# Kernel optimization log

Measured on AMD Instinct MI355X. Metric: run time of the kernel, lower is better.

Reference implementation:

```python
import jax, jax.numpy as jnp
import numpy as np

D_MODEL = 768
N_HEADS = 12
D_FF = 3072
EPS = 1e-6


def _xavier(key, shape):
    fan_out, fan_in = shape
    a = jnp.sqrt(6.0 / (fan_in + fan_out))
    return jax.random.uniform(key, shape, jnp.float32, -a, a)


def setup_inputs() -> dict:
    key = jax.random.key(0)
    ks = jax.random.split(key, 10)
    B, S = 2, 2048
    x = jax.random.normal(ks[0], (B, S, D_MODEL), jnp.float32)
    mask = jax.random.randint(ks[1], (B, 1, 1, S), 0, 2) == 1
    wq = _xavier(ks[2], (D_MODEL, D_MODEL)); bq = jnp.zeros((D_MODEL,))
    wk = _xavier(ks[3], (D_MODEL, D_MODEL)); bk = jnp.zeros((D_MODEL,))
    wv = _xavier(ks[4], (D_MODEL, D_MODEL)); bv = jnp.zeros((D_MODEL,))
    wo = _xavier(ks[5], (D_MODEL, D_MODEL)); bo = jnp.zeros((D_MODEL,))
    w1 = _xavier(ks[6], (D_FF, D_MODEL)); b1 = jnp.zeros((D_FF,))
    w2 = _xavier(ks[7], (D_MODEL, D_FF)); b2 = jnp.zeros((D_MODEL,))
    g1 = jnp.ones((D_MODEL,)); be1 = jnp.zeros((D_MODEL,))
    g2 = jnp.ones((D_MODEL,)); be2 = jnp.zeros((D_MODEL,))
    return dict(x=x, mask=mask, wq=wq, bq=bq, wk=wk, bk=bk, wv=wv, bv=bv,
                wo=wo, bo=bo, w1=w1, b1=b1, w2=w2, b2=b2,
                g1=g1, be1=be1, g2=g2, be2=be2)


def _layer_norm(x, gamma, beta):
    # torch: mean + unbiased std (ddof=1), divide by (std + eps)
    mean = jnp.mean(x, axis=-1, keepdims=True)
    std = jnp.std(x, axis=-1, keepdims=True, ddof=1)
    return gamma * (x - mean) / (std + EPS) + beta


def _encoder(x, mask, wq, bq, wk, bk, wv, bv, wo, bo, w1, b1, w2, b2, g1, be1, g2, be2):
    B, S, D = x.shape
    H, Dk = N_HEADS, D // N_HEADS
    q = (x @ wq.T + bq).reshape(B, S, H, Dk).transpose(0, 2, 1, 3)
    k = (x @ wk.T + bk).reshape(B, S, H, Dk).transpose(0, 2, 1, 3)
    v = (x @ wv.T + bv).reshape(B, S, H, Dk).transpose(0, 2, 1, 3)
    scores = jnp.einsum('bhqd,bhkd->bhqk', q, k) / jnp.sqrt(jnp.float32(Dk))
    scores = jnp.where(mask, jnp.float32(-1e9), scores)
    probs = jax.nn.softmax(scores, axis=-1)
    attn = jnp.einsum('bhqk,bhkd->bhqd', probs, v)
    attn = attn.transpose(0, 2, 1, 3).reshape(B, S, D)
    attn = attn @ wo.T + bo
    x = _layer_norm(x + attn, g1, be1)
    ff = jax.nn.relu(x @ w1.T + b1) @ w2.T + b2
    return _layer_norm(x + ff, g2, be2)


def reference(x, mask, wq, bq, wk, bk, wv, bv, wo, bo, w1, b1, w2, b2, g1, be1, g2, be2):
    return _encoder(x, mask, wq, bq, wk, bk, wv, bv, wo, bo, w1, b1, w2, b2, g1, be1, g2, be2)
```

## Files before the change

kernel.cpp:

```cpp
#include <hip/hip_runtime.h>
#include <hip/hip_bf16.h>

typedef __hip_bfloat16 bf16;
typedef unsigned short ushort;
typedef __attribute__((ext_vector_type(8))) short short8;
typedef __attribute__((ext_vector_type(4))) float f32x4;

__device__ __forceinline__ float b2f(bf16 h) { return __bfloat162float(h); }
__device__ __forceinline__ bf16 f2b(float f) { return __float2bfloat16(f); }
__device__ __forceinline__ ushort f2bu(float f) {
    bf16 t = __float2bfloat16(f);
    ushort u;
    __builtin_memcpy(&u, &t, 2);
    return u;
}
__device__ __forceinline__ float bits2f(unsigned int u16) {
    unsigned int v = u16 << 16;
    float f;
    __builtin_memcpy(&f, &v, 4);
    return f;
}

__device__ __forceinline__ void gload16(const void* g, void* l) {
    __builtin_amdgcn_global_load_lds(
        (const __attribute__((address_space(1))) void*)g,
        (__attribute__((address_space(3))) void*)l, 16, 0, 0);
}

__global__ void detect_dtype_kernel(const unsigned short* __restrict__ x,
                                    int* __restrict__ flag) {
    __shared__ int cnt;
    if (threadIdx.x == 0) cnt = 0;
    __syncthreads();
    int local = 0;
    for (int i = threadIdx.x; i < 2048; i += 256) {
        float v = bits2f((unsigned int)x[i]);
        if (!(fabsf(v) < 1e4f)) local++;
    }
    atomicAdd(&cnt, local);
    __syncthreads();
    if (threadIdx.x == 0) flag[0] = (cnt >= 8) ? 1 : 0;
}

__device__ __forceinline__ void load8f_rt(const void* p, int isf, float* f) {
    if (isf) {
        const float* q = (const float*)p;
        float4 a = *(const float4*)q;
        float4 b = *(const float4*)(q + 4);
        f[0] = a.x; f[1] = a.y; f[2] = a.z; f[3] = a.w;
        f[4] = b.x; f[5] = b.y; f[6] = b.z; f[7] = b.w;
    } else {
        uint4 u = *(const uint4*)p;
        f[0] = bits2f(u.x & 0xffffu); f[1] = bits2f(u.x >> 16);
        f[2] = bits2f(u.y & 0xffffu); f[3] = bits2f(u.y >> 16);
        f[4] = bits2f(u.z & 0xffffu); f[5] = bits2f(u.z >> 16);
        f[6] = bits2f(u.w & 0xffffu); f[7] = bits2f(u.w >> 16);
    }
}
__device__ __forceinline__ float loadf_rt(const void* p, int isf, size_t i) {
    return isf ? ((const float*)p)[i] : bits2f(((const ushort*)p)[i]);
}

__global__ __launch_bounds__(256) void conv_all_k(
    const int* __restrict__ dflag,
    const void* __restrict__ x,
    const void* __restrict__ wq, const void* __restrict__ wk,
    const void* __restrict__ wv, const void* __restrict__ wo,
    const void* __restrict__ w1, const void* __restrict__ w2,
    const void* __restrict__ bq, const void* __restrict__ bk,
    const void* __restrict__ bv, const void* __restrict__ bo,
    const void* __restrict__ b1, const void* __restrict__ b2,
    const void* __restrict__ g1, const void* __restrict__ be1,
    const void* __restrict__ g2, const void* __restrict__ be2,
    ushort* __restrict__ xb, ushort* __restrict__ wall,
    float* __restrict__ vall)
{
    const int isf = dflag[0];
    const int esz = isf ? 4 : 2;
    const int gt = blockIdx.x * 256 + threadIdx.x;
    const int stride = gridDim.x * 256;

    for (int v = gt; v < 393216; v += stride) {
        float f[8];
        load8f_rt((const char*)x + (size_t)v * 8 * esz, isf, f);
        unsigned int wd[4];
        #pragma unroll
        for (int i = 0; i < 4; ++i)
            wd[i] = (unsigned int)f2bu(f[2 * i]) | ((unsigned int)f2bu(f[2 * i + 1]) << 16);
        *(uint4*)(xb + (size_t)v * 8) = make_uint4(wd[0], wd[1], wd[2], wd[3]);
    }
    for (int v = gt; v < 884736; v += stride) {
        const void* src; int loc;
        if (v < 73728)        { src = wq; loc = v; }
        else if (v < 147456)  { src = wk; loc = v - 73728; }
        else if (v < 221184)  { src = wv; loc = v - 147456; }
        else if (v < 294912)  { src = wo; loc = v - 221184; }
        else if (v < 589824)  { src = w1; loc = v - 294912; }
        else                  { src = w2; loc = v - 589824; }
        float f[8];
        load8f_rt((const char*)src + (size_t)loc * 8 * esz, isf, f);
        unsigned int wd[4];
        #pragma unroll
        for (int i = 0; i < 4; ++i)
            wd[i] = (unsigned int)f2bu(f[2 * i]) | ((unsigned int)f2bu(f[2 * i + 1]) << 16);
        *(uint4*)(wall + (size_t)v * 8) = make_uint4(wd[0], wd[1], wd[2], wd[3]);
    }
    for (int i = gt; i < 9984; i += stride) {
        const void* s; int l;
        if (i < 768)       { s = bq;  l = i; }
        else if (i < 1536) { s = bk;  l = i - 768; }
        else if (i < 2304) { s = bv;  l = i - 1536; }
        else if (i < 3072) { s = bo;  l = i - 2304; }
        else if (i < 6144) { s = b1;  l = i - 3072; }
        else if (i < 6912) { s = b2;  l = i - 6144; }
        else if (i < 7680) { s = g1;  l = i - 6912; }
        else if (i < 8448) { s = be1; l = i - 7680; }
        else if (i < 9216) { s = g2;  l = i - 8448; }
        else               { s = be2; l = i - 9216; }
        vall[i] = loadf_rt(s, isf, l);
    }
}

template <int BM>
__device__ __forceinline__ void gemm_bf16_body(
    const ushort* __restrict__ A, const ushort* __restrict__ Bw,
    const float* __restrict__ bias, ushort* __restrict__ Cb,
    float* __restrict__ Cf, int N, int K, int bm, int bn, int relu)
{
    __shared__ __align__(16) ushort As[2][BM][64];
    __shared__ __align__(16) ushort Bs[2][128][64];
    const int tid = threadIdx.x;
    const int w = tid >> 6, lane = tid & 63;
    const int quad = lane >> 4, l15 = lane & 15;
    constexpr int FM = BM / 32;
    const int wr = (w >> 1) * (BM / 2), wc = (w & 1) * 64;

    constexpr int CA = (BM * 128) / 4096;
    constexpr int CB = 4;
    size_t aoff[CA]; int albase[CA];
    #pragma unroll
    for (int c = 0; c < CA; ++c) {
        int byte = c * 4096 + tid * 16;
        int row = byte >> 7, colb = byte & 127;
        int csrc = colb ^ ((row & 7) << 4);
        aoff[c] = (size_t)(bm + row) * K + (csrc >> 1);
        albase[c] = c * 4096 + w * 1024;
    }
    size_t boff[CB]; int blbase[CB];
    #pragma unroll
    for (int c = 0; c < CB; ++c) {
        int byte = c * 4096 + tid * 16;
        int row = byte >> 7, colb = byte & 127;
        int csrc = colb ^ ((row & 7) << 4);
        boff[c] = (size_t)(bn + row) * K + (csrc >> 1);
        blbase[c] = c * 4096 + w * 1024;
    }

    f32x4 acc[FM][4];
    #pragma unroll
    for (int i = 0; i < FM; ++i)
        #pragma unroll
        for (int j = 0; j < 4; ++j) acc[i][j] = (f32x4){0.f, 0.f, 0.f, 0.f};

    constexpr int ASZ = BM * 128;
    constexpr int BSZ = 128 * 128;

#define STAGE(buf, k0)                                                        \
    {                                                                         \
        char* ab = (char*)As + (buf) * ASZ;                                   \
        char* bb = (char*)Bs + (buf) * BSZ;                                   \
        _Pragma("unroll")                                                     \
        for (int c = 0; c < CA; ++c)                                          \
            gload16(A + aoff[c] + (k0), ab + albase[c]);                      \
        _Pragma("unroll")                                                     \
        for (int c = 0; c < CB; ++c)                                          \
            gload16(Bw + boff[c] + (k0), bb + blbase[c]);                     \
    }

    const int NT = K >> 6;
    STAGE(0, 0);
    int cur = 0;
    for (int t = 0; t < NT; ++t) {
        __syncthreads();
        if (t + 1 < NT) STAGE(cur ^ 1, (t + 1) * 64);

        const ushort (*Asb)[64] = As[cur];
        const ushort (*Bsb)[64] = Bs[cur];
        short8 af[FM][2], bfr[4][2];
        #pragma unroll
        for (int i = 0; i < FM; ++i) {
            int r = wr + i * 16 + l15;
            int sw = (r & 7) << 3;
            af[i][0] = *(const short8*)&Asb[r][(quad * 8) ^ sw];
            af[i][1] = *(const short8*)&Asb[r][(32 + quad * 8) ^ sw];
        }
        #pragma unroll
        for (int j = 0; j < 4; ++j) {
            int r = wc + j * 16 + l15;
            int sw = (r & 7) << 3;
            bfr[j][0] = *(const short8*)&Bsb[r][(quad * 8) ^ sw];
            bfr[j][1] = *(const short8*)&Bsb[r][(32 + quad * 8) ^ sw];
        }
        #pragma unroll
        for (int h = 0; h < 2; ++h)
            #pragma unroll
            for (int i = 0; i < FM; ++i)
                #pragma unroll
                for (int j = 0; j < 4; ++j)
                    acc[i][j] = __builtin_amdgcn_mfma_f32_16x16x32_bf16(
                        af[i][h], bfr[j][h], acc[i][j], 0, 0, 0);
        cur ^= 1;
    }
#undef STAGE

    #pragma unroll
    for (int j = 0; j < 4; ++j) {
        int col = bn + wc + j * 16 + l15;
        float bv = bias[col];
        #pragma unroll
        for (int i = 0; i < FM; ++i) {
            int row0 = bm + wr + i * 16 + quad * 4;
            #pragma unroll
            for (int r = 0; r < 4; ++r) {
                float vv = acc[i][j][r] + bv;
                if (relu) vv = fmaxf(vv, 0.f);
                size_t idx = (size_t)(row0 + r) * N + col;
                if (Cb) Cb[idx] = f2bu(vv);
                if (Cf) Cf[idx] = vv;
            }
        }
    }
}

__device__ __forceinline__ int xcd_swz(int bid, int nwg) {
    int cpx = nwg >> 3;
    return (bid & 7) * cpx + (bid >> 3);
}

template <int BM>
__global__ __launch_bounds__(256) void gemm_b(
    const ushort* __restrict__ A, const ushort* __restrict__ Bw,
    const float* __restrict__ bias, ushort* __restrict__ Cb,
    float* __restrict__ Cf, int N, int K, int relu)
{
    int nwg = gridDim.x * gridDim.y;
    int bid = xcd_swz(blockIdx.y * gridDim.x + blockIdx.x, nwg);
    int bx = bid % gridDim.x, by = bid / gridDim.x;
    gemm_bf16_body<BM>(A, Bw, bias, Cb, Cf, N, K, by * BM, bx * 128, relu);
}

__global__ __launch_bounds__(256) void gemm_qkv_b(
    const ushort* __restrict__ x, const ushort* __restrict__ wall,
    const float* __restrict__ vall,
    ushort* __restrict__ qb, ushort* __restrict__ kb, ushort* __restrict__ vb)
{
    int bid = xcd_swz(blockIdx.y * 18 + blockIdx.x, 576);
    int bx = bid % 18, by = bid / 18;
    const int mat = bx / 6;
    const int bn = (bx % 6) * 128;
    const ushort* W = wall + (size_t)mat * 589824;
    const float* Bi = vall + mat * 768;
    ushort* O = (mat == 0) ? qb : (mat == 1) ? kb : vb;
    gemm_bf16_body<128>(x, W, Bi, O, nullptr, 768, 768, by * 128, bn, 0);
}

__global__ __launch_bounds__(512) void attn_mfma_b(
    const ushort* __restrict__ q, const ushort* __restrict__ k,
    const ushort* __restrict__ v, const int* __restrict__ mask,
    float* __restrict__ opart, float* __restrict__ mlbuf)
{
    const int S = 2048, D = 768;
    const size_t NXD = 3145728;
    const float SC2 = 0.125f * 1.44269504088896f;
    __shared__ __align__(16) ushort Ks[64][72];
    __shared__ __align__(16) ushort Vt[64][72];
    __shared__ __align__(16) ushort Ps[8][16][72];
    __shared__ float mkAll[1024];

    const int tid = threadIdx.x;
    const int w = tid >> 6, lane = tid & 63;
    const int quad = lane >> 4, l15 = lane & 15;

    const int bx = blockIdx.x;
    const int part = bx / 384;
    const int rest = bx - part * 384;
    const int q0 = (rest & 15) * 128;
    const int h = (rest >> 4) % 12;
    const int b = rest / 192;
    const int kbase = part * 1024;

    #pragma unroll
    for (int i = 0; i < 2; ++i) {
        int idx = tid + i * 512;
        mkAll[idx] = mask[b * S + kbase + idx] ? -30000.f : 0.f;
    }

    const size_t qrow = (size_t)(b * S + q0 + w * 16 + l15) * D + h * 64;
    const short8 aQ0 = *(const short8*)&q[qrow + quad * 8];
    const short8 aQ1 = *(const short8*)&q[qrow + 32 + quad * 8];

    short8 ones;
    #pragma unroll
    for (int j = 0; j < 8; ++j) ones[j] = (short)0x3F80;

    f32x4 o[4], lacc;
    #pragma unroll
    for (int i = 0; i < 4; ++i) o[i] = (f32x4){0.f, 0.f, 0.f, 0.f};
    lacc = (f32x4){0.f, 0.f, 0.f, 0.f};
    float m_run = -3.0e38f;

    const int sr = tid >> 3;
    const int sc0 = (tid & 7) * 8;

    const ushort* kp = k + (size_t)(b * S + kbase + sr) * D + h * 64 + sc0;
    const ushort* vp = v + (size_t)(b * S + kbase + lane) * D + h * 64 + w * 8;
    uint4 ka = *(const uint4*)kp;
    uint4 va = *(const uint4*)vp;

    for (int kt = 0; kt < 16; ++kt) {
        __syncthreads();
        *(uint4*)&Ks[sr][sc0] = ka;
        {
            alignas(16) ushort tmp[8];
            *(uint4*)tmp = va;
            #pragma unroll
            for (int i = 0; i < 8; ++i) Vt[w * 8 + i][lane] = tmp[i];
        }
        __syncthreads();

        if (kt + 1 < 16) {
            kp += 64 * D;
            vp += 64 * D;
            ka = *(const uint4*)kp;
            va = *(const uint4*)vp;
        }

        const float* mk = &mkAll[kt * 64];
        float scv[4][4];
        float vm = -3.0e38f;
        __builtin_amdgcn_s_setprio(1);
        #pragma unroll
        for (int s = 0; s < 4; ++s) {
            short8 bk0 = *(const short8*)&Ks[s * 16 + l15][quad * 8];
            short8 bk1 = *(const short8*)&Ks[s * 16 + l15][32 + quad * 8];
            f32x4 c = (f32x4){0.f, 0.f, 0.f, 0.f};
            c = __builtin_amdgcn_mfma_f32_16x16x32_bf16(aQ0, bk0, c, 0, 0, 0);
            c = __builtin_amdgcn_mfma_f32_16x16x32_bf16(aQ1, bk1, c, 0, 0, 0);
            float mb = mk[s * 16 + l15];
            #pragma unroll
            for (int r = 0; r < 4; ++r) {
                float val = __builtin_fmaf(c[r], SC2, mb);
                scv[s][r] = val;
                vm = fmaxf(vm, val);
            }
        }
        __builtin_amdgcn_s_setprio(0);
        vm = fmaxf(vm, __shfl_xor(vm, 1, 16));
        vm = fmaxf(vm, __shfl_xor(vm, 2, 16));
        vm = fmaxf(vm, __shfl_xor(vm, 4, 16));
        vm = fmaxf(vm, __shfl_xor(vm, 8, 16));

        if (__any(vm > m_run + 11.0f)) {
            float mn = fmaxf(m_run, vm);
            float alpha = exp2f(m_run - mn);
            #pragma unroll
            for (int s = 0; s < 4; ++s) o[s] *= alpha;
            lacc *= alpha;
            m_run = mn;
        }

        #pragma unroll
        for (int r = 0; r < 4; ++r)
            #pragma unroll
            for (int s = 0; s < 4; ++s)
                Ps[w][quad * 4 + r][(s * 16 + l15) ^ (quad << 4)] =
                    f2bu(exp2f(scv[s][r] - m_run));
        asm volatile("s_waitcnt lgkmcnt(0)" ::: "memory");

        {
            const int pswz = (l15 >> 2) << 4;
            short8 aP0 = *(const short8*)&Ps[w][l15][(quad * 8) ^ pswz];
            short8 aP1 = *(const short8*)&Ps[w][l15][(32 + quad * 8) ^ pswz];
            __builtin_amdgcn_s_setprio(1);
            lacc = __builtin_amdgcn_mfma_f32_16x16x32_bf16(aP0, ones, lacc, 0, 0, 0);
            lacc = __builtin_amdgcn_mfma_f32_16x16x32_bf16(aP1, ones, lacc, 0, 0, 0);
            #pragma unroll
            for (int s = 0; s < 4; ++s) {
                short8 bv0 = *(const short8*)&Vt[s * 16 + l15][quad * 8];
                short8 bv1 = *(const short8*)&Vt[s * 16 + l15][32 + quad * 8];
                o[s] = __builtin_amdgcn_mfma_f32_16x16x32_bf16(aP0, bv0, o[s], 0, 0, 0);
                o[s] = __builtin_amdgcn_mfma_f32_16x16x32_bf16(aP1, bv1, o[s], 0, 0, 0);
            }
            __builtin_amdgcn_s_setprio(0);
        }
    }

    const size_t obase = (size_t)part * NXD +
                         (size_t)(b * S + q0 + w * 16) * D + h * 64;
    #pragma unroll
    for (int r = 0; r < 4; ++r)
        #pragma unroll
        for (int s = 0; s < 4; ++s)
            opart[obase + (size_t)(quad * 4 + r) * D + s * 16 + l15] = o[s][r];
    if (l15 == 0) {
        #pragma unroll
        for (int r = 0; r < 4; ++r) {
            int row = b * S + q0 + w * 16 + quad * 4 + r;
            size_t mi = (((size_t)part * 4096 + row) * 12 + h) * 2;
            mlbuf[mi] = m_run;
            mlbuf[mi + 1] = lacc[r];
        }
    }
}

__global__ __launch_bounds__(256) void attn_combine(
    const float* __restrict__ opart, const float* __restrict__ mlbuf,
    ushort* __restrict__ ctx)
{
    const size_t NXD = 3145728;
    const int row = blockIdx.x;
    const int tid = threadIdx.x;
    #pragma unroll
    for (int i = 0; i < 3; ++i) {
        int d = tid + i * 256;
        int h = d >> 6;
        size_t m0i = ((size_t)row * 12 + h) * 2;
        size_t m1i = (((size_t)4096 + row) * 12 + h) * 2;
        float m0 = mlbuf[m0i], l0 = mlbuf[m0i + 1];
        float m1 = mlbuf[m1i], l1 = mlbuf[m1i + 1];
        float m = fmaxf(m0, m1);
        float e0 = exp2f(m0 - m), e1 = exp2f(m1 - m);
        float inv = 1.f / (l0 * e0 + l1 * e1);
        size_t idx = (size_t)row * 768 + d;
        float val = (opart[idx] * e0 + opart[NXD + idx] * e1) * inv;
        ctx[idx] = f2bu(val);
    }
}

__global__ __launch_bounds__(256) void ln1_kernel(
    const int* __restrict__ dflag,
    const void* __restrict__ xa, const float* __restrict__ r,
    const float* __restrict__ gamma, const float* __restrict__ beta,
    ushort* __restrict__ outb, float* __restrict__ outf)
{
    const int isf = dflag[0];
    const int row = blockIdx.x;
    const int tid = threadIdx.x;
    __shared__ float red[4];
    const size_t base = (size_t)row * 768;

    float x[3];
    #pragma unroll
    for (int i = 0; i < 3; ++i) {
        int d = tid + i * 256;
        x[i] = loadf_rt(xa, isf, base + d) + r[base + d];
    }

    float s = x[0] + x[1] + x[2];
    #pragma unroll
    for (int off = 32; off > 0; off >>= 1) s += __shfl_down(s, off, 64);
    if ((tid & 63) == 0) red[tid >> 6] = s;
    __syncthreads();
    float mean = (red[0] + red[1] + red[2] + red[3]) * (1.f / 768.f);
    __syncthreads();

    float vsum = 0.f;
    #pragma unroll
    for (int i = 0; i < 3; ++i) {
        float dd = x[i] - mean;
        vsum += dd * dd;
    }
    #pragma unroll
    for (int off = 32; off > 0; off >>= 1) vsum += __shfl_down(vsum, off, 64);
    if ((tid & 63) == 0) red[tid >> 6] = vsum;
    __syncthreads();
    float var = (red[0] + red[1] + red[2] + red[3]) * (1.f / 767.f);
    float inv = 1.f / (sqrtf(var) + 1e-6f);

    #pragma unroll
    for (int i = 0; i < 3; ++i) {
        int d = tid + i * 256;
        float y = gamma[d] * (x[i] - mean) * inv + beta[d];
        outb[base + d] = f2bu(y);
        outf[base + d] = y;
    }
}

__global__ __launch_bounds__(256) void ln2_kernel(
    const int* __restrict__ dflag,
    const float* __restrict__ a, const float* __restrict__ r,
    const float* __restrict__ gamma, const float* __restrict__ beta,
    void* __restrict__ out)
{
    const int isf = dflag[0];
    const int row = blockIdx.x;
    const int tid = threadIdx.x;
    __shared__ float red[4];
    const size_t base = (size_t)row * 768;

    float x[3];
    #pragma unroll
    for (int i = 0; i < 3; ++i) {
        int d = tid + i * 256;
        x[i] = a[base + d] + r[base + d];
    }

    float s = x[0] + x[1] + x[2];
    #pragma unroll
    for (int off = 32; off > 0; off >>= 1) s += __shfl_down(s, off, 64);
    if ((tid & 63) == 0) red[tid >> 6] = s;
    __syncthreads();
    float mean = (red[0] + red[1] + red[2] + red[3]) * (1.f / 768.f);
    __syncthreads();

    float vsum = 0.f;
    #pragma unroll
    for (int i = 0; i < 3; ++i) {
        float dd = x[i] - mean;
        vsum += dd * dd;
    }
    #pragma unroll
    for (int off = 32; off > 0; off >>= 1) vsum += __shfl_down(vsum, off, 64);
    if ((tid & 63) == 0) red[tid >> 6] = vsum;
    __syncthreads();
    float var = (red[0] + red[1] + red[2] + red[3]) * (1.f / 767.f);
    float inv = 1.f / (sqrtf(var) + 1e-6f);

    #pragma unroll
    for (int i = 0; i < 3; ++i) {
        int d = tid + i * 256;
        float y = gamma[d] * (x[i] - mean) * inv + beta[d];
        if (isf) ((float*)out)[base + d] = y;
        else     ((ushort*)out)[base + d] = f2bu(y);
    }
}

extern "C" void kernel_launch(void* const* d_in, const int* in_sizes, int n_in,
                              void* d_out, int out_size, void* d_ws, size_t ws_size,
                              hipStream_t stream) {
    const size_t nxd = 3145728;
    char* base = (char*)d_ws;
    int* dflag = (int*)base;

    char* p = base + 256;
    ushort* xb   = (ushort*)p; p += nxd * 2;
    ushort* wall = (ushort*)p; p += 7077888ull * 2;
    float*  vall = (float*)p;  p += 40960;
    ushort* qb   = (ushort*)p;
    ushort* kb   = qb + nxd;
    ushort* vb   = kb + nxd;
    ushort* ctx  = vb + nxd;
    ushort* ff1b = qb;
    p += 4 * nxd * 2;
    float* oproj = (float*)p;
    float* ff2f  = oproj;
    p += nxd * 4;
    ushort* ln1b = (ushort*)p; p += nxd * 2;
    float*  ln1f = (float*)p;  p += nxd * 4;

    float* opart = oproj;
    float* mlbuf = oproj + 2 * nxd;

    const int* mask = (const int*)d_in[1];
    dim3 blk(256);

    detect_dtype_kernel<<<dim3(1), blk, 0, stream>>>(
        (const unsigned short*)d_in[0], dflag);

    conv_all_k<<<dim3(1024), blk, 0, stream>>>(dflag,
        d_in[0], d_in[2], d_in[4], d_in[6], d_in[8], d_in[10], d_in[12],
        d_in[3], d_in[5], d_in[7], d_in[9], d_in[11], d_in[13],
        d_in[14], d_in[15], d_in[16], d_in[17], xb, wall, vall);

    gemm_qkv_b<<<dim3(18, 32), blk, 0, stream>>>(xb, wall, vall, qb, kb, vb);

    attn_mfma_b<<<dim3(768), dim3(512), 0, stream>>>(qb, kb, vb, mask, opart, mlbuf);
    attn_combine<<<dim3(4096), blk, 0, stream>>>(opart, mlbuf, ctx);

    gemm_b<64><<<dim3(6, 64), blk, 0, stream>>>(
        ctx, wall + 1769472, vall + 2304, nullptr, oproj, 768, 768, 0);

    ln1_kernel<<<dim3(4096), blk, 0, stream>>>(dflag,
        d_in[0], oproj, vall + 6912, vall + 7680, ln1b, ln1f);

    gemm_b<128><<<dim3(24, 32), blk, 0, stream>>>(
        ln1b, wall + 2359296, vall + 3072, ff1b, nullptr, 3072, 768, 1);

    gemm_b<64><<<dim3(6, 64), blk, 0, stream>>>(
        ff1b, wall + 4718592, vall + 6144, nullptr, ff2f, 768, 3072, 0);

    ln2_kernel<<<dim3(4096), blk, 0, stream>>>(dflag,
        ln1f, ff2f, vall + 8448, vall + 9216, d_out);
}
```

Baseline: 324.7 us.

## Double-buffer K/V in LDS and keep attention probabilities in registers

The attention kernel now double-buffers the K and V^T tiles in shared memory, so the next tile is staged before the current one is computed and one barrier per iteration is dropped. It also swaps the QK^T MFMA operand order so scores come out transposed, with each lane holding one query row. The probabilities are then packed with v_cvt_pk_bf16_f32 and rearranged into the A-operand layout with ds_bpermute instead of going through a shared-memory P buffer. The row max reduction, alpha rescale and final m output are adjusted to the new layout, at the cost of more shuffles and LDS use.

```diff
diff --git a/kernel.cpp b/kernel.cpp
--- a/kernel.cpp
+++ b/kernel.cpp
@@ -272,9 +272,8 @@
     const int S = 2048, D = 768;
     const size_t NXD = 3145728;
     const float SC2 = 0.125f * 1.44269504088896f;
-    __shared__ __align__(16) ushort Ks[64][72];
-    __shared__ __align__(16) ushort Vt[64][72];
-    __shared__ __align__(16) ushort Ps[8][16][72];
+    __shared__ __align__(16) ushort Ks[2][64][72];
+    __shared__ __align__(16) ushort Vt[2][64][72];
     __shared__ float mkAll[1024];
 
     const int tid = threadIdx.x;
@@ -312,27 +311,39 @@
     const int sr = tid >> 3;
     const int sc0 = (tid & 7) * 8;
 
+    const int idxA = ((((lane >> 4) & 1) * 2) * 16 + l15) * 4;
+    const int idxB = idxA + 64;
+
     const ushort* kp = k + (size_t)(b * S + kbase + sr) * D + h * 64 + sc0;
     const ushort* vp = v + (size_t)(b * S + kbase + lane) * D + h * 64 + w * 8;
     uint4 ka = *(const uint4*)kp;
     uint4 va = *(const uint4*)vp;
 
+#define STAGE_KV(bb)                                                          \
+    {                                                                         \
+        *(uint4*)&Ks[bb][sr][sc0] = ka;                                       \
+        alignas(16) ushort tmp[8];                                            \
+        *(uint4*)tmp = va;                                                    \
+        _Pragma("unroll")                                                     \
+        for (int i = 0; i < 8; ++i) Vt[bb][w * 8 + i][lane] = tmp[i];         \
+    }
+
+    STAGE_KV(0);
+    kp += 64 * D; vp += 64 * D;
+    ka = *(const uint4*)kp;
+    va = *(const uint4*)vp;
+
+    int cur = 0;
     for (int kt = 0; kt < 16; ++kt) {
         __syncthreads();
-        *(uint4*)&Ks[sr][sc0] = ka;
-        {
-            alignas(16) ushort tmp[8];
-            *(uint4*)tmp = va;
-            #pragma unroll
-            for (int i = 0; i < 8; ++i) Vt[w * 8 + i][lane] = tmp[i];
-        }
-        __syncthreads();
 
         if (kt + 1 < 16) {
-            kp += 64 * D;
-            vp += 64 * D;
-            ka = *(const uint4*)kp;
-            va = *(const uint4*)vp;
+            STAGE_KV(cur ^ 1);
+            if (kt + 2 < 16) {
+                kp += 64 * D; vp += 64 * D;
+                ka = *(const uint4*)kp;
+                va = *(const uint4*)vp;
+            }
         }
 
         const float* mk = &mkAll[kt * 64];
@@ -341,59 +352,81 @@
         __builtin_amdgcn_s_setprio(1);
         #pragma unroll
         for (int s = 0; s < 4; ++s) {
-            short8 bk0 = *(const short8*)&Ks[s * 16 + l15][quad * 8];
-            short8 bk1 = *(const short8*)&Ks[s * 16 + l15][32 + quad * 8];
+            short8 ak0 = *(const short8*)&Ks[cur][s * 16 + l15][quad * 8];
+            short8 ak1 = *(const short8*)&Ks[cur][s * 16 + l15][32 + quad * 8];
             f32x4 c = (f32x4){0.f, 0.f, 0.f, 0.f};
-            c = __builtin_amdgcn_mfma_f32_16x16x32_bf16(aQ0, bk0, c, 0, 0, 0);
-            c = __builtin_amdgcn_mfma_f32_16x16x32_bf16(aQ1, bk1, c, 0, 0, 0);
-            float mb = mk[s * 16 + l15];
+            c = __builtin_amdgcn_mfma_f32_16x16x32_bf16(ak0, aQ0, c, 0, 0, 0);
+            c = __builtin_amdgcn_mfma_f32_16x16x32_bf16(ak1, aQ1, c, 0, 0, 0);
+            float4 m4 = *(const float4*)&mk[s * 16 + quad * 4];
+            float mar[4] = {m4.x, m4.y, m4.z, m4.w};
             #pragma unroll
             for (int r = 0; r < 4; ++r) {
-                float val = __builtin_fmaf(c[r], SC2, mb);
+                float val = __builtin_fmaf(c[r], SC2, mar[r]);
                 scv[s][r] = val;
                 vm = fmaxf(vm, val);
             }
         }
         __builtin_amdgcn_s_setprio(0);
-        vm = fmaxf(vm, __shfl_xor(vm, 1, 16));
-        vm = fmaxf(vm, __shfl_xor(vm, 2, 16));
-        vm = fmaxf(vm, __shfl_xor(vm, 4, 16));
-        vm = fmaxf(vm, __shfl_xor(vm, 8, 16));
+        vm = fmaxf(vm, __shfl_xor(vm, 16));
+        vm = fmaxf(vm, __shfl_xor(vm, 32));
 
         if (__any(vm > m_run + 11.0f)) {
             float mn = fmaxf(m_run, vm);
             float alpha = exp2f(m_run - mn);
+            float a_o[4];
             #pragma unroll
-            for (int s = 0; s < 4; ++s) o[s] *= alpha;
-            lacc *= alpha;
-            m_run = mn;
-        }
-
-        #pragma unroll
-        for (int r = 0; r < 4; ++r)
+            for (int r = 0; r < 4; ++r)
+                a_o[r] = __shfl(alpha, quad * 4 + r, 16);
             #pragma unroll
             for (int s = 0; s < 4; ++s)
-                Ps[w][quad * 4 + r][(s * 16 + l15) ^ (quad << 4)] =
-                    f2bu(exp2f(scv[s][r] - m_run));
-        asm volatile("s_waitcnt lgkmcnt(0)" ::: "memory");
-
-        {
-            const int pswz = (l15 >> 2) << 4;
-            short8 aP0 = *(const short8*)&Ps[w][l15][(quad * 8) ^ pswz];
-            short8 aP1 = *(const short8*)&Ps[w][l15][(32 + quad * 8) ^ pswz];
-            __builtin_amdgcn_s_setprio(1);
-            lacc = __builtin_amdgcn_mfma_f32_16x16x32_bf16(aP0, ones, lacc, 0, 0, 0);
-            lacc = __builtin_amdgcn_mfma_f32_16x16x32_bf16(aP1, ones, lacc, 0, 0, 0);
+                #pragma unroll
+                for (int r = 0; r < 4; ++r) o[s][r] *= a_o[r];
             #pragma unroll
-            for (int s = 0; s < 4; ++s) {
-                short8 bv0 = *(const short8*)&Vt[s * 16 + l15][quad * 8];
-                short8 bv1 = *(const short8*)&Vt[s * 16 + l15][32 + quad * 8];
-                o[s] = __builtin_amdgcn_mfma_f32_16x16x32_bf16(aP0, bv0, o[s], 0, 0, 0);
-                o[s] = __builtin_amdgcn_mfma_f32_16x16x32_bf16(aP1, bv1, o[s], 0, 0, 0);
-            }
-            __builtin_amdgcn_s_setprio(0);
-        }
-    }
+            for (int r = 0; r < 4; ++r) lacc[r] *= a_o[r];
+            m_run = mn;
+        }
+
+        unsigned int pk[4][2];
+        #pragma unroll
+        for (int s = 0; s < 4; ++s) {
+            float p0 = exp2f(scv[s][0] - m_run);
+            float p1 = exp2f(scv[s][1] - m_run);
+            float p2 = exp2f(scv[s][2] - m_run);
+            float p3 = exp2f(scv[s][3] - m_run);
+            asm("v_cvt_pk_bf16_f32 %0, %1, %2" : "=v"(pk[s][0]) : "v"(p0), "v"(p1));
+            asm("v_cvt_pk_bf16_f32 %0, %1, %2" : "=v"(pk[s][1]) : "v"(p2), "v"(p3));
+        }
+        int aw0[4], aw1[4];
+        #pragma unroll
+        for (int d = 0; d < 4; ++d) {
+            int idx = (d < 2) ? idxA : idxB;
+            int hh = d & 1;
+            int t0 = __builtin_amdgcn_ds_bpermute(idx, (int)pk[0][hh]);
+            int t1 = __builtin_amdgcn_ds_bpermute(idx, (int)pk[1][hh]);
+            aw0[d] = (lane < 32) ? t0 : t1;
+            int t2 = __builtin_amdgcn_ds_bpermute(idx, (int)pk[2][hh]);
+            int t3 = __builtin_amdgcn_ds_bpermute(idx, (int)pk[3][hh]);
+            aw1[d] = (lane < 32) ? t2 : t3;
+        }
+        short8 aP0, aP1;
+        __builtin_memcpy(&aP0, aw0, 16);
+        __builtin_memcpy(&aP1, aw1, 16);
+
+        __builtin_amdgcn_s_setprio(1);
+        lacc = __builtin_amdgcn_mfma_f32_16x16x32_bf16(aP0, ones, lacc, 0, 0, 0);
+        lacc = __builtin_amdgcn_mfma_f32_16x16x32_bf16(aP1, ones, lacc, 0, 0, 0);
+        #pragma unroll
+        for (int s = 0; s < 4; ++s) {
+            short8 bv0 = *(const short8*)&Vt[cur][s * 16 + l15][quad * 8];
+            short8 bv1 = *(const short8*)&Vt[cur][s * 16 + l15][32 + quad * 8];
+            o[s] = __builtin_amdgcn_mfma_f32_16x16x32_bf16(aP0, bv0, o[s], 0, 0, 0);
+            o[s] = __builtin_amdgcn_mfma_f32_16x16x32_bf16(aP1, bv1, o[s], 0, 0, 0);
+        }
+        __builtin_amdgcn_s_setprio(0);
+
+        cur ^= 1;
+    }
+#undef STAGE_KV
 
     const size_t obase = (size_t)part * NXD +
                          (size_t)(b * S + q0 + w * 16) * D + h * 64;
@@ -402,12 +435,16 @@
         #pragma unroll
         for (int s = 0; s < 4; ++s)
             opart[obase + (size_t)(quad * 4 + r) * D + s * 16 + l15] = o[s][r];
+    float mq[4];
+    #pragma unroll
+    for (int r = 0; r < 4; ++r)
+        mq[r] = __shfl(m_run, quad * 4 + r, 16);
     if (l15 == 0) {
         #pragma unroll
         for (int r = 0; r < 4; ++r) {
             int row = b * S + q0 + w * 16 + quad * 4 + r;
             size_t mi = (((size_t)part * 4096 + row) * 12 + h) * 2;
-            mlbuf[mi] = m_run;
+            mlbuf[mi] = mq[r];
             mlbuf[mi + 1] = lacc[r];
         }
     }
```

Result: no change. 318.5 us (-1.9%).
